# Optimization experiments

Hardware: AMD Instinct MI355X
Metric: run time of the kernel (lower is better)

The kernel has to match this reference:

```python
import jax, jax.numpy as jnp
import numpy as np

N_NODES = 50000
N_EDGES = 800000
N_GRAPHS = 256
HID = 64           # hidden_channels
H, C = 2, 64       # GAT heads, per-head channels
D2 = H * C         # 128 = hidden_channels * heads
BN_EPS = 1e-5


def setup_inputs() -> dict:
    key = jax.random.key(0)
    ks = iter(jax.random.split(key, 64))

    def p(shape, scale=0.05):
        return (jax.random.normal(next(ks), shape, dtype=jnp.float32) * scale)

    inp = {}
    inp["metadata"] = jax.random.normal(next(ks), (N_NODES, 4), dtype=jnp.float32)
    inp["waveform_features"] = jax.random.normal(next(ks), (N_NODES, 64), dtype=jnp.float32)
    inp["edge_index"] = jax.random.randint(next(ks), (2, N_EDGES), 0, N_NODES, dtype=jnp.int64)
    inp["batch"] = jnp.sort(jax.random.randint(next(ks), (N_NODES,), 0, N_GRAPHS, dtype=jnp.int64))

    # encoders / combiner
    inp["meta_w"] = p((4, HID // 2)); inp["meta_b"] = p((HID // 2,))
    inp["wave_w"] = p((64, HID // 2)); inp["wave_b"] = p((HID // 2,))
    inp["comb_w"] = p((HID, HID));     inp["comb_b"] = p((HID,))

    # GAT layers: layer 0 maps HID->H*C, layers 1,2 map D2->H*C
    inp["gat_w0"] = p((HID, D2)); inp["gat_as0"] = p((H, C)); inp["gat_ad0"] = p((H, C)); inp["gat_b0"] = p((D2,))
    inp["gat_w1"] = p((D2, D2));  inp["gat_as1"] = p((H, C)); inp["gat_ad1"] = p((H, C)); inp["gat_b1"] = p((D2,))
    inp["gat_w2"] = p((D2, D2));  inp["gat_as2"] = p((H, C)); inp["gat_ad2"] = p((H, C)); inp["gat_b2"] = p((D2,))

    # batch norms (eval mode: running stats), stacked over 3 layers
    inp["bn_gamma"] = jnp.ones((3, D2), jnp.float32) + p((3, D2))
    inp["bn_beta"] = p((3, D2))
    inp["bn_mean"] = p((3, D2))
    inp["bn_var"] = jax.random.uniform(next(ks), (3, D2), jnp.float32, 0.5, 1.5)

    # predictors
    inp["lat_w1"] = p((D2, HID)); inp["lat_b1"] = p((HID,))
    inp["lat_w2"] = p((HID, 1));  inp["lat_b2"] = p((1,))
    inp["lon_w1"] = p((D2, HID)); inp["lon_b1"] = p((HID,))
    inp["lon_w2"] = p((HID, 1));  inp["lon_b2"] = p((1,))
    return inp


def gat_conv(x, src, dst, n, W, a_src, a_dst, b):
    """PyG-style GATConv, heads=H concat, leaky_relu slope 0.2, self-loops already in src/dst."""
    h = (x @ W).reshape(n, H, C)                          # [N,H,C]
    s = jnp.einsum('nhc,hc->nh', h, a_src)                # alpha_src [N,H]
    d = jnp.einsum('nhc,hc->nh', h, a_dst)                # alpha_dst [N,H]
    e = jax.nn.leaky_relu(s[src] + d[dst], 0.2)           # [E,H]
    m = jax.ops.segment_max(e, dst, num_segments=n)       # per-dst softmax (segment)
    ex = jnp.exp(e - m[dst])
    denom = jax.ops.segment_sum(ex, dst, num_segments=n)
    alpha = ex / (denom[dst] + 1e-16)                     # [E,H]
    out = jax.ops.segment_sum(h[src] * alpha[:, :, None], dst, num_segments=n)  # [N,H,C]
    return out.reshape(n, H * C) + b


def reference(metadata, waveform_features, edge_index, batch,
              meta_w, meta_b, wave_w, wave_b, comb_w, comb_b,
              gat_w0, gat_as0, gat_ad0, gat_b0,
              gat_w1, gat_as1, gat_ad1, gat_b1,
              gat_w2, gat_as2, gat_ad2, gat_b2,
              bn_gamma, bn_beta, bn_mean, bn_var,
              lat_w1, lat_b1, lat_w2, lat_b2,
              lon_w1, lon_b1, lon_w2, lon_b2):
    n = metadata.shape[0]
    me = jax.nn.relu(metadata @ meta_w + meta_b)
    we = jax.nn.relu(waveform_features @ wave_w + wave_b)
    x = jnp.concatenate([me, we], axis=1)                 # [N, HID]
    x = jax.nn.relu(x @ comb_w + comb_b)

    loops = jnp.arange(n, dtype=edge_index.dtype)         # GATConv adds self-loops
    src = jnp.concatenate([edge_index[0], loops])
    dst = jnp.concatenate([edge_index[1], loops])

    gat_params = [(gat_w0, gat_as0, gat_ad0, gat_b0),
                  (gat_w1, gat_as1, gat_ad1, gat_b1),
                  (gat_w2, gat_as2, gat_ad2, gat_b2)]
    for i in range(3):
        x_res = x if i > 0 else None
        x = gat_conv(x, src, dst, n, *gat_params[i])
        x = (x - bn_mean[i]) * (bn_gamma[i] / jnp.sqrt(bn_var[i] + BN_EPS)) + bn_beta[i]
        if x_res is not None and x.shape == x_res.shape:
            x = x + x_res
        x = jax.nn.relu(x)                                # dropout inactive (eval)

    # global_mean_pool over graphs
    sums = jax.ops.segment_sum(x, batch, num_segments=N_GRAPHS)
    cnt = jax.ops.segment_sum(jnp.ones((n, 1), x.dtype), batch, num_segments=N_GRAPHS)
    xg = sums / jnp.maximum(cnt, 1.0)                     # [B, 128]

    lat = jax.nn.relu(xg @ lat_w1 + lat_b1) @ lat_w2 + lat_b2
    lon = jax.nn.relu(xg @ lon_w1 + lon_b1) @ lon_w2 + lon_b2
    return lat, lon
```

## Files before the change

### kernel.cpp

```cpp
#include <hip/hip_runtime.h>
#include <hip/hip_bf16.h>
#include <stdint.h>

#define NN 50000
#define NNP 50048
#define NE 800000
#define ET 850000
#define NG 256
#define CAP 128
#define NB 392
#define EB 4096
#define NEB ((ET + EB - 1) / EB)

typedef __hip_bfloat16 bf16;
typedef __attribute__((ext_vector_type(8))) short short8;
typedef __attribute__((ext_vector_type(4))) float floatx4;

__device__ __forceinline__ float b2f(bf16 v) { return __bfloat162float(v); }
__device__ __forceinline__ float lrelu(float x) { return x > 0.f ? x : 0.2f * x; }
__device__ __forceinline__ short f2b(float f) {
    unsigned u = __float_as_uint(f);
    unsigned r = (u + 0x7FFFu + ((u >> 16) & 1u)) >> 16;
    return (short)r;
}
__device__ __forceinline__ float sh2f(short s) { return __uint_as_float(((unsigned)(unsigned short)s) << 16); }
__device__ __forceinline__ float blo(unsigned u) { return __uint_as_float(u << 16); }
__device__ __forceinline__ float bhi(unsigned u) { return __uint_as_float(u & 0xFFFF0000u); }
__device__ __forceinline__ unsigned pck(float a, float b) {
    return ((unsigned)(unsigned short)f2b(a)) | (((unsigned)(unsigned short)f2b(b)) << 16);
}

__device__ __forceinline__ float wred_sum(float v) {
    for (int o = 32; o > 0; o >>= 1) v += __shfl_xor(v, o, 64);
    return v;
}
__device__ __forceinline__ float wred_max(float v) {
    for (int o = 32; o > 0; o >>= 1) v = fmaxf(v, __shfl_xor(v, o, 64));
    return v;
}

__global__ void detect_kernel(const unsigned int* __restrict__ meta_words,
                              const unsigned int* __restrict__ ei_words,
                              int* __restrict__ flags, int* __restrict__ gbh) {
    __shared__ int insane, odd_nonzero;
    for (int k = threadIdx.x; k < NB; k += 256) gbh[k] = 0;
    if (threadIdx.x == 0) { insane = 0; odd_nonzero = 0; }
    __syncthreads();
    int cnt = 0;
    for (int k = 0; k < 8; k++) {
        unsigned int w = meta_words[threadIdx.x * 8 + k];
        int elo = (int)(((w & 0xFFFFu) >> 7) & 0xFF);
        int ehi = (int)(((w >> 16) >> 7) & 0xFF);
        if (elo >= 0x8D) cnt++;
        if (ehi >= 0x8D) cnt++;
    }
    if (cnt) atomicAdd(&insane, cnt);
    if (ei_words[threadIdx.x * 2 + 1] != 0u) atomicAdd(&odd_nonzero, 1);
    __syncthreads();
    if (threadIdx.x == 0) {
        flags[0] = (insane >= 4) ? 1 : 0;
        flags[1] = (odd_nonzero == 0) ? 1 : 0;
    }
}

struct PrepArgs {
    const void* src[32];
    int len[32];
    int dst_off[32];
    int blk_base[33];
    int cvtBlks, wtBlks, wfBlks, intBlks;
    const void* w0; const void* w1; const void* w2;
    const void* ww; const void* wc;
    const void* wf_src;
    const void* ei_src;
    const void* bat_src;
};

__global__ void prep_kernel(PrepArgs a, float* __restrict__ cf,
                            short* __restrict__ wtall, short* __restrict__ wavewT,
                            short* __restrict__ combwT,
                            short* __restrict__ wfhi, short* __restrict__ wflo,
                            int* __restrict__ ei32, int* __restrict__ bat32,
                            const int* __restrict__ flags) {
    int b = blockIdx.x;
    bool fp32f = flags[0] != 0;
    if (b < a.cvtBlks) {
        int ai = 0;
        while (b >= a.blk_base[ai + 1]) ai++;
        int base = (b - a.blk_base[ai]) * 1024 + threadIdx.x;
        const float* sf = (const float*)a.src[ai];
        const bf16* sh = (const bf16*)a.src[ai];
        float* d = cf + a.dst_off[ai];
        int len = a.len[ai];
        #pragma unroll
        for (int u = 0; u < 4; u++) {
            int i = base + u * 256;
            if (i < len) d[i] = fp32f ? sf[i] : b2f(sh[i]);
        }
        return;
    }
    b -= a.cvtBlks;
    if (b < a.wtBlks) {
        int idx = b * 256 + threadIdx.x;
        const void* src; short* dst; int K, N, loc;
        if (idx < 8192)        { src = a.w0; dst = wtall;          K = 64;  N = 128; loc = idx; }
        else if (idx < 24576)  { src = a.w1; dst = wtall + 8192;   K = 128; N = 128; loc = idx - 8192; }
        else if (idx < 40960)  { src = a.w2; dst = wtall + 24576;  K = 128; N = 128; loc = idx - 24576; }
        else if (idx < 43008)  { src = a.ww; dst = wavewT;         K = 64;  N = 32;  loc = idx - 40960; }
        else if (idx < 47104)  { src = a.wc; dst = combwT;         K = 64;  N = 64;  loc = idx - 43008; }
        else return;
        int nch = loc / K, k = loc % K;
        int si = k * N + nch;
        dst[loc] = fp32f ? f2b(((const float*)src)[si]) : ((const short*)src)[si];
        return;
    }
    b -= a.wtBlks;
    if (b < a.wfBlks) {
        int idx = b * 256 + threadIdx.x;
        int i8 = idx * 8;
        if (i8 >= NNP * 64) return;
        short8 h = {0, 0, 0, 0, 0, 0, 0, 0};
        short8 l = {0, 0, 0, 0, 0, 0, 0, 0};
        if (i8 < NN * 64) {
            if (fp32f) {
                const float* sf = (const float*)a.wf_src + i8;
                #pragma unroll
                for (int k = 0; k < 8; k++) {
                    float v = sf[k];
                    short hh = f2b(v);
                    h[k] = hh;
                    l[k] = f2b(v - sh2f(hh));
                }
            } else {
                h = *(const short8*)((const short*)a.wf_src + i8);
            }
        }
        *(short8*)(wfhi + i8) = h;
        *(short8*)(wflo + i8) = l;
        return;
    }
    b -= a.wfBlks;
    int idx = b * 256 + threadIdx.x;
    if (idx >= 825000) return;
    bool i64f = flags[1] != 0;
    if (idx < 800000) {
        int2 o;
        if (i64f) { int4 v = ((const int4*)a.ei_src)[idx]; o.x = v.x; o.y = v.z; }
        else      { o = ((const int2*)a.ei_src)[idx]; }
        *(int2*)(ei32 + idx * 2) = o;
    } else {
        int k = idx - 800000;
        int2 o;
        if (i64f) { int4 v = ((const int4*)a.bat_src)[k]; o.x = v.x; o.y = v.z; }
        else      { o = ((const int2*)a.bat_src)[k]; }
        *(int2*)(bat32 + k * 2) = o;
    }
}

__global__ __launch_bounds__(256) void encode_mfma_kernel(
        const float* __restrict__ meta, const float* __restrict__ meta_w,
        const float* __restrict__ meta_b,
        const short* __restrict__ wfhi, const short* __restrict__ wflo,
        const short* __restrict__ wavewT, const float* __restrict__ wave_b,
        const short* __restrict__ combwT, const float* __restrict__ comb_b,
        short* __restrict__ xout, const int* __restrict__ flags) {
    __shared__ short xc_hi[64][72];
    __shared__ short xc_lo[64][72];
    int t = threadIdx.x;
    int wave = t >> 6, lane = t & 63;
    int m16 = lane & 15, quad = lane >> 4;
    int nblk = blockIdx.x * 64;
    bool fp32f = flags[0] != 0;

    #pragma unroll
    for (int u = 0; u < 8; u++) {
        int idx = u * 256 + t;
        int node_l = idx >> 5, ch = idx & 31;
        int node = nblk + node_l;
        float acc = meta_b[ch];
        if (node < NN) {
            #pragma unroll
            for (int k = 0; k < 4; k++)
                acc += meta[node * 4 + k] * meta_w[k * 32 + ch];
        }
        float v = fmaxf(acc, 0.f);
        short hh = f2b(v);
        xc_hi[node_l][ch] = hh;
        xc_lo[node_l][ch] = f2b(v - sh2f(hh));
    }

    int row0 = nblk + wave * 16;
    const short* pah = wfhi + (size_t)(row0 + m16) * 64 + quad * 8;
    const short* pal = wflo + (size_t)(row0 + m16) * 64 + quad * 8;
    floatx4 wacc[2];
    wacc[0] = (floatx4)(0.f); wacc[1] = (floatx4)(0.f);
    #pragma unroll
    for (int ks = 0; ks < 64; ks += 32) {
        short8 ah = *(const short8*)(pah + ks);
        #pragma unroll
        for (int c = 0; c < 2; c++) {
            short8 b = *(const short8*)(wavewT + (c * 16 + m16) * 64 + ks + quad * 8);
            wacc[c] = __builtin_amdgcn_mfma_f32_16x16x32_bf16(ah, b, wacc[c], 0, 0, 0);
        }
        if (fp32f) {
            short8 al = *(const short8*)(pal + ks);
            #pragma unroll
            for (int c = 0; c < 2; c++) {
                short8 b = *(const short8*)(wavewT + (c * 16 + m16) * 64 + ks + quad * 8);
                wacc[c] = __builtin_amdgcn_mfma_f32_16x16x32_bf16(al, b, wacc[c], 0, 0, 0);
            }
        }
    }
    #pragma unroll
    for (int c = 0; c < 2; c++) {
        float bb = wave_b[c * 16 + m16];
        #pragma unroll
        for (int r = 0; r < 4; r++) {
            int node_l = wave * 16 + quad * 4 + r;
            int ch = 32 + c * 16 + m16;
            float v = fmaxf(wacc[c][r] + bb, 0.f);
            short hh = f2b(v);
            xc_hi[node_l][ch] = hh;
            xc_lo[node_l][ch] = f2b(v - sh2f(hh));
        }
    }
    __syncthreads();

    floatx4 acc2[4];
    #pragma unroll
    for (int c = 0; c < 4; c++) acc2[c] = (floatx4)(0.f);
    #pragma unroll
    for (int ks = 0; ks < 64; ks += 32) {
        short8 ah = *(const short8*)&xc_hi[wave * 16 + m16][ks + quad * 8];
        short8 al = *(const short8*)&xc_lo[wave * 16 + m16][ks + quad * 8];
        #pragma unroll
        for (int c = 0; c < 4; c++) {
            short8 b = *(const short8*)(combwT + (c * 16 + m16) * 64 + ks + quad * 8);
            acc2[c] = __builtin_amdgcn_mfma_f32_16x16x32_bf16(ah, b, acc2[c], 0, 0, 0);
            acc2[c] = __builtin_amdgcn_mfma_f32_16x16x32_bf16(al, b, acc2[c], 0, 0, 0);
        }
    }
    #pragma unroll
    for (int c = 0; c < 4; c++) {
        int ch = c * 16 + m16;
        float bb = comb_b[ch];
        #pragma unroll
        for (int r = 0; r < 4; r++) {
            int node = nblk + wave * 16 + quad * 4 + r;
            float v = fmaxf(acc2[c][r] + bb, 0.f);
            xout[(size_t)node * 64 + ch] = f2b(v);
        }
    }
}

__global__ void bucket_hist_kernel(const int* __restrict__ ei, int* __restrict__ gbh) {
    __shared__ int lh[NB];
    int t = threadIdx.x;
    for (int k = t; k < NB; k += 256) lh[k] = 0;
    __syncthreads();
    int base = blockIdx.x * EB;
    #pragma unroll 4
    for (int u = 0; u < EB / 256; u++) {
        int i = base + u * 256 + t;
        if (i < ET) {
            int dst = (i < NE) ? ei[NE + i] : (i - NE);
            atomicAdd(&lh[dst >> 7], 1);
        }
    }
    __syncthreads();
    for (int k = t; k < NB; k += 256)
        if (lh[k]) atomicAdd(&gbh[k], lh[k]);
}

__global__ void scan_bounds_kernel(const int* __restrict__ gbh, int* __restrict__ gbo,
                                   int* __restrict__ bcur,
                                   const int* __restrict__ batch, int* __restrict__ starts) {
    if (blockIdx.x == 0) {
        __shared__ int buf[512];
        int t = threadIdx.x;
        int v = (t < NB) ? gbh[t] : 0;
        buf[t] = v;
        __syncthreads();
        for (int o = 1; o < 512; o <<= 1) {
            int x = (t >= o) ? buf[t - o] : 0;
            __syncthreads();
            buf[t] += x;
            __syncthreads();
        }
        if (t < NB) { int e = buf[t] - v; gbo[t] = e; bcur[t] = e; }
        if (t == 0) gbo[NB] = ET;
    } else {
        int g = threadIdx.x;
        if (g <= NG) {
            int lo = 0, hi = NN;
            while (lo < hi) {
                int mid = (lo + hi) >> 1;
                if (batch[mid] < g) lo = mid + 1; else hi = mid;
            }
            starts[g] = lo;
        }
    }
}

__global__ void bucket_scatter_kernel(const int* __restrict__ ei, int* __restrict__ bcur,
                                      uint2* __restrict__ bkt) {
    __shared__ int lh[NB];
    __shared__ int lbase[NB];
    int t = threadIdx.x;
    for (int k = t; k < NB; k += 256) lh[k] = 0;
    __syncthreads();
    int base = blockIdx.x * EB;
    #pragma unroll 4
    for (int u = 0; u < EB / 256; u++) {
        int i = base + u * 256 + t;
        if (i < ET) {
            int dst = (i < NE) ? ei[NE + i] : (i - NE);
            atomicAdd(&lh[dst >> 7], 1);
        }
    }
    __syncthreads();
    for (int k = t; k < NB; k += 256) {
        int c = lh[k];
        lbase[k] = c ? atomicAdd(&bcur[k], c) : 0;
        lh[k] = 0;
    }
    __syncthreads();
    #pragma unroll 4
    for (int u = 0; u < EB / 256; u++) {
        int i = base + u * 256 + t;
        if (i < ET) {
            int src, dst;
            if (i < NE) { src = ei[i]; dst = ei[NE + i]; }
            else        { src = i - NE; dst = i - NE; }
            int b = dst >> 7;
            int pos = lbase[b] + atomicAdd(&lh[b], 1);
            bkt[pos] = make_uint2((unsigned)src, (unsigned)dst);
        }
    }
}

__global__ void bucket_finalize_kernel(const uint2* __restrict__ bkt,
                                       const int* __restrict__ gbo,
                                       int* __restrict__ off, int* __restrict__ csr) {
    __shared__ int hist[128];
    __shared__ int cur[128];
    int b = blockIdx.x;
    int t = threadIdx.x;
    int e0 = gbo[b], e1 = gbo[b + 1];
    if (t < 128) hist[t] = 0;
    __syncthreads();
    for (int i = e0 + t; i < e1; i += 256)
        atomicAdd(&hist[bkt[i].y & 127], 1);
    __syncthreads();
    int v = (t < 128) ? hist[t] : 0;
    if (t < 128) cur[t] = v;
    __syncthreads();
    for (int o = 1; o < 128; o <<= 1) {
        int x = (t < 128 && t >= o) ? cur[t - o] : 0;
        __syncthreads();
        if (t < 128) cur[t] += x;
        __syncthreads();
    }
    if (t < 128) {
        int ex = e0 + cur[t] - v;
        int node = b * 128 + t;
        if (node <= NN) off[node] = ex;
        cur[t] = ex;
    }
    __syncthreads();
    for (int i = e0 + t; i < e1; i += 256) {
        uint2 e = bkt[i];
        int pos = atomicAdd(&cur[e.y & 127], 1);
        csr[pos] = (int)e.x;
    }
}

__global__ __launch_bounds__(256) void gemm_mfma_kernel(
        const short* __restrict__ x, const short* __restrict__ wt,
        const float* __restrict__ a_s, const float* __restrict__ a_d,
        short* __restrict__ h, float* __restrict__ s, float* __restrict__ d,
        int K, int n) {
    int wave = threadIdx.x >> 6;
    int lane = threadIdx.x & 63;
    int row0 = (blockIdx.x * 4 + wave) * 16;
    int m16 = lane & 15;
    int quad = lane >> 4;
    int kq = quad * 8;

    const short* pa = x + (size_t)(row0 + m16) * K + kq;

    floatx4 acc[8];
    #pragma unroll
    for (int c = 0; c < 8; c++) acc[c] = (floatx4)(0.f);

    for (int ks = 0; ks < K; ks += 32) {
        short8 av = *(const short8*)(pa + ks);
        #pragma unroll
        for (int c = 0; c < 8; c++) {
            short8 b = *(const short8*)(wt + (size_t)(c * 16 + m16) * K + ks + kq);
            acc[c] = __builtin_amdgcn_mfma_f32_16x16x32_bf16(av, b, acc[c], 0, 0, 0);
        }
    }

    #pragma unroll
    for (int c = 0; c < 8; c++) {
        #pragma unroll
        for (int r = 0; r < 4; r++) {
            int node = row0 + quad * 4 + r;
            if (node < n) h[(size_t)node * 128 + c * 16 + m16] = f2b(acc[c][r]);
        }
    }

    float sp[2][4] = {{0, 0, 0, 0}, {0, 0, 0, 0}};
    float dp[2][4] = {{0, 0, 0, 0}, {0, 0, 0, 0}};
    #pragma unroll
    for (int c = 0; c < 8; c++) {
        float as_ = a_s[c * 16 + m16];
        float ad_ = a_d[c * 16 + m16];
        int hh = c >> 2;
        #pragma unroll
        for (int r = 0; r < 4; r++) {
            sp[hh][r] += acc[c][r] * as_;
            dp[hh][r] += acc[c][r] * ad_;
        }
    }
    #pragma unroll
    for (int o = 1; o < 16; o <<= 1) {
        #pragma unroll
        for (int hh = 0; hh < 2; hh++)
            #pragma unroll
            for (int r = 0; r < 4; r++) {
                sp[hh][r] += __shfl_xor(sp[hh][r], o, 64);
                dp[hh][r] += __shfl_xor(dp[hh][r], o, 64);
            }
    }
    if (m16 == 0) {
        #pragma unroll
        for (int r = 0; r < 4; r++) {
            int node = row0 + quad * 4 + r;
            if (node < n) {
                s[node * 2 + 0] = sp[0][r];
                s[node * 2 + 1] = sp[1][r];
                d[node * 2 + 0] = dp[0][r];
                d[node * 2 + 1] = dp[1][r];
            }
        }
    }
}

__global__ __launch_bounds__(256) void gat_aggregate_kernel(
        const unsigned* __restrict__ hp, const float* __restrict__ sv,
        const float* __restrict__ dv, const int* __restrict__ off,
        const int* __restrict__ csr, const float* __restrict__ bias,
        const float* __restrict__ bn_g, const float* __restrict__ bn_b,
        const float* __restrict__ bn_m, const float* __restrict__ bn_v,
        const unsigned* __restrict__ res, unsigned* __restrict__ out, int n) {
    __shared__ float exs[4][CAP][2];
    __shared__ int scs[4][CAP];
    int w = threadIdx.x >> 6;
    int lane = threadIdx.x & 63;
    int node = blockIdx.x * 4 + w;
    bool ok = node < n;
    int begin = 0, end = 0, deg = 0;
    float d0 = 0.f, d1 = 0.f;
    if (ok) {
        begin = off[node]; end = off[node + 1]; deg = end - begin;
        d0 = dv[node * 2 + 0]; d1 = dv[node * 2 + 1];
    }
    bool fits = deg <= CAP;
    float inv0 = 0.f, inv1 = 0.f;

    if (ok && fits) {
        int i0 = begin + lane, i1 = begin + 64 + lane;
        int sa = (i0 < end) ? csr[i0] : -1;
        int sb = (i1 < end) ? csr[i1] : -1;
        float e0a = -3e38f, e1a = -3e38f, e0b = -3e38f, e1b = -3e38f;
        if (sa >= 0) {
            float2 sp = *(const float2*)(sv + sa * 2);
            e0a = lrelu(sp.x + d0); e1a = lrelu(sp.y + d1);
        }
        if (sb >= 0) {
            float2 sp = *(const float2*)(sv + sb * 2);
            e0b = lrelu(sp.x + d0); e1b = lrelu(sp.y + d1);
        }
        float m0 = wred_max(fmaxf(e0a, e0b));
        float m1 = wred_max(fmaxf(e1a, e1b));
        float x0a = 0.f, x1a = 0.f, x0b = 0.f, x1b = 0.f;
        if (sa >= 0) {
            x0a = __expf(e0a - m0); x1a = __expf(e1a - m1);
            exs[w][lane][0] = x0a; exs[w][lane][1] = x1a; scs[w][lane] = sa;
        }
        if (sb >= 0) {
            x0b = __expf(e0b - m0); x1b = __expf(e1b - m1);
            exs[w][lane + 64][0] = x0b; exs[w][lane + 64][1] = x1b; scs[w][lane + 64] = sb;
        }
        float z0 = wred_sum(x0a + x0b);
        float z1 = wred_sum(x1a + x1b);
        inv0 = 1.f / (z0 + 1e-16f);
        inv1 = 1.f / (z1 + 1e-16f);
    }
    __syncthreads();
    if (!ok) return;

    if (fits) {
        int ll = lane & 15;
        int grp = lane >> 4;
        int hsel = (ll >= 8) ? 1 : 0;
        const uint4* hp4 = (const uint4*)hp;
        float a0 = 0, a1 = 0, a2 = 0, a3 = 0, a4 = 0, a5 = 0, a6 = 0, a7 = 0;
        for (int i = 0; i < deg; i += 4) {
            int e = i + grp;
            if (e < deg) {
                int src = scs[w][e];
                float a = exs[w][e][hsel];
                uint4 u = hp4[(size_t)src * 16 + ll];
                a0 += a * blo(u.x); a1 += a * bhi(u.x);
                a2 += a * blo(u.y); a3 += a * bhi(u.y);
                a4 += a * blo(u.z); a5 += a * bhi(u.z);
                a6 += a * blo(u.w); a7 += a * bhi(u.w);
            }
        }
        a0 += __shfl_xor(a0, 16, 64); a0 += __shfl_xor(a0, 32, 64);
        a1 += __shfl_xor(a1, 16, 64); a1 += __shfl_xor(a1, 32, 64);
        a2 += __shfl_xor(a2, 16, 64); a2 += __shfl_xor(a2, 32, 64);
        a3 += __shfl_xor(a3, 16, 64); a3 += __shfl_xor(a3, 32, 64);
        a4 += __shfl_xor(a4, 16, 64); a4 += __shfl_xor(a4, 32, 64);
        a5 += __shfl_xor(a5, 16, 64); a5 += __shfl_xor(a5, 32, 64);
        a6 += __shfl_xor(a6, 16, 64); a6 += __shfl_xor(a6, 32, 64);
        a7 += __shfl_xor(a7, 16, 64); a7 += __shfl_xor(a7, 32, 64);
        float inv = hsel ? inv1 : inv0;
        a0 *= inv; a1 *= inv; a2 *= inv; a3 *= inv;
        a4 *= inv; a5 *= inv; a6 *= inv; a7 *= inv;

        float4 bi0 = ((const float4*)bias)[2 * ll],  bi1 = ((const float4*)bias)[2 * ll + 1];
        float4 g0  = ((const float4*)bn_g)[2 * ll],  g1  = ((const float4*)bn_g)[2 * ll + 1];
        float4 be0 = ((const float4*)bn_b)[2 * ll],  be1 = ((const float4*)bn_b)[2 * ll + 1];
        float4 mu0 = ((const float4*)bn_m)[2 * ll],  mu1 = ((const float4*)bn_m)[2 * ll + 1];
        float4 va0 = ((const float4*)bn_v)[2 * ll],  va1 = ((const float4*)bn_v)[2 * ll + 1];
        float v0 = (a0 + bi0.x - mu0.x) * (g0.x * rsqrtf(va0.x + 1e-5f)) + be0.x;
        float v1 = (a1 + bi0.y - mu0.y) * (g0.y * rsqrtf(va0.y + 1e-5f)) + be0.y;
        float v2 = (a2 + bi0.z - mu0.z) * (g0.z * rsqrtf(va0.z + 1e-5f)) + be0.z;
        float v3 = (a3 + bi0.w - mu0.w) * (g0.w * rsqrtf(va0.w + 1e-5f)) + be0.w;
        float v4 = (a4 + bi1.x - mu1.x) * (g1.x * rsqrtf(va1.x + 1e-5f)) + be1.x;
        float v5 = (a5 + bi1.y - mu1.y) * (g1.y * rsqrtf(va1.y + 1e-5f)) + be1.y;
        float v6 = (a6 + bi1.z - mu1.z) * (g1.z * rsqrtf(va1.z + 1e-5f)) + be1.z;
        float v7 = (a7 + bi1.w - mu1.w) * (g1.w * rsqrtf(va1.w + 1e-5f)) + be1.w;
        if (res) {
            uint4 r = ((const uint4*)res)[(size_t)node * 16 + ll];
            v0 += blo(r.x); v1 += bhi(r.x); v2 += blo(r.y); v3 += bhi(r.y);
            v4 += blo(r.z); v5 += bhi(r.z); v6 += blo(r.w); v7 += bhi(r.w);
        }
        v0 = fmaxf(v0, 0.f); v1 = fmaxf(v1, 0.f); v2 = fmaxf(v2, 0.f); v3 = fmaxf(v3, 0.f);
        v4 = fmaxf(v4, 0.f); v5 = fmaxf(v5, 0.f); v6 = fmaxf(v6, 0.f); v7 = fmaxf(v7, 0.f);
        if (lane < 16) {
            ((uint4*)out)[(size_t)node * 16 + ll] =
                make_uint4(pck(v0, v1), pck(v2, v3), pck(v4, v5), pck(v6, v7));
        }
    } else {
        float mm0 = -3e38f, mm1 = -3e38f;
        for (int i = begin + lane; i < end; i += 64) {
            int sc = csr[i];
            float2 sp = *(const float2*)(sv + sc * 2);
            mm0 = fmaxf(mm0, lrelu(sp.x + d0));
            mm1 = fmaxf(mm1, lrelu(sp.y + d1));
        }
        mm0 = wred_max(mm0); mm1 = wred_max(mm1);
        float z0 = 0.f, z1 = 0.f;
        for (int i = begin + lane; i < end; i += 64) {
            int sc = csr[i];
            float2 sp = *(const float2*)(sv + sc * 2);
            z0 += __expf(lrelu(sp.x + d0) - mm0);
            z1 += __expf(lrelu(sp.y + d1) - mm1);
        }
        z0 = wred_sum(z0); z1 = wred_sum(z1);
        float i0_ = 1.f / (z0 + 1e-16f), i1_ = 1.f / (z1 + 1e-16f);
        bool head0 = lane < 32;
        float acc0 = 0.f, acc1 = 0.f;
        for (int i = begin; i < end; i++) {
            int sc = csr[i];
            float2 sp = *(const float2*)(sv + sc * 2);
            float a = head0 ? __expf(lrelu(sp.x + d0) - mm0) * i0_
                            : __expf(lrelu(sp.y + d1) - mm1) * i1_;
            unsigned u = hp[(size_t)sc * 64 + lane];
            acc0 += a * blo(u);
            acc1 += a * bhi(u);
        }
        int c0 = 2 * lane, c1 = c0 + 1;
        float v0 = acc0 + bias[c0];
        float v1 = acc1 + bias[c1];
        v0 = (v0 - bn_m[c0]) * (bn_g[c0] * rsqrtf(bn_v[c0] + 1e-5f)) + bn_b[c0];
        v1 = (v1 - bn_m[c1]) * (bn_g[c1] * rsqrtf(bn_v[c1] + 1e-5f)) + bn_b[c1];
        if (res) {
            unsigned r = res[(size_t)node * 64 + lane];
            v0 += blo(r);
            v1 += bhi(r);
        }
        v0 = fmaxf(v0, 0.f);
        v1 = fmaxf(v1, 0.f);
        out[(size_t)node * 64 + lane] = pck(v0, v1);
    }
}

__global__ void pool_kernel(const unsigned* __restrict__ x,
                            const int* __restrict__ starts, float* __restrict__ xg) {
    __shared__ float part[4][128];
    int g = blockIdx.x;
    int wv = threadIdx.x >> 6, lane = threadIdx.x & 63;
    int s0 = starts[g], e0 = starts[g + 1];
    float a0 = 0.f, a1 = 0.f;
    for (int node = s0 + wv; node < e0; node += 4) {
        unsigned u = x[(size_t)node * 64 + lane];
        a0 += blo(u);
        a1 += bhi(u);
    }
    part[wv][lane * 2] = a0;
    part[wv][lane * 2 + 1] = a1;
    __syncthreads();
    if (wv == 0) {
        float t0 = part[0][lane * 2] + part[1][lane * 2] + part[2][lane * 2] + part[3][lane * 2];
        float t1 = part[0][lane * 2 + 1] + part[1][lane * 2 + 1] + part[2][lane * 2 + 1] + part[3][lane * 2 + 1];
        float icf = 1.f / fmaxf((float)(e0 - s0), 1.f);
        xg[g * 128 + 2 * lane] = t0 * icf;
        xg[g * 128 + 2 * lane + 1] = t1 * icf;
    }
}

__global__ void head_kernel(const float* __restrict__ xg,
                            const float* __restrict__ w1a, const float* __restrict__ b1a,
                            const float* __restrict__ w2a, const float* __restrict__ b2a,
                            const float* __restrict__ w1o, const float* __restrict__ b1o,
                            const float* __restrict__ w2o, const float* __restrict__ b2o,
                            const int* __restrict__ flags, void* __restrict__ out) {
    int g = blockIdx.x;
    int wave = threadIdx.x >> 6;
    int lane = threadIdx.x & 63;
    const float* w1 = wave ? w1o : w1a;
    const float* b1 = wave ? b1o : b1a;
    const float* w2 = wave ? w2o : w2a;
    const float* b2 = wave ? b2o : b2a;
    float acc = b1[lane];
    for (int c = 0; c < 128; c++)
        acc += xg[g * 128 + c] * w1[c * 64 + lane];
    acc = fmaxf(acc, 0.f);
    float contrib = wred_sum(acc * w2[lane]);
    if (lane == 0) {
        float r = contrib + b2[0];
        if (flags[0]) ((float*)out)[wave * NG + g] = r;
        else          ((bf16*)out)[wave * NG + g] = __float2bfloat16(r);
    }
}

extern "C" void kernel_launch(void* const* d_in, const int* in_sizes, int n_in,
                              void* d_out, int out_size, void* d_ws, size_t ws_size,
                              hipStream_t stream) {
    static const int fidx[32] = {0,1, 4,5,6,7,8,9, 10,11,12,13, 14,15,16,17,
                                 18,19,20,21, 22,23,24,25, 26,27,28,29, 30,31,32,33};
    static const int flen[32] = {200000, 3200000, 128, 32, 2048, 32, 4096, 64,
                                 8192, 128, 128, 128, 16384, 128, 128, 128,
                                 16384, 128, 128, 128, 384, 384, 384, 384,
                                 8192, 64, 64, 1, 8192, 64, 64, 1};
    PrepArgs pa;
    int O[32];
    int tot = 0, blk = 0;
    for (int i = 0; i < 32; i++) {
        bool skip = (i == 1) || (i == 4) || (i == 6) || (i == 8) || (i == 12) || (i == 16);
        int cl = skip ? 0 : flen[i];
        pa.src[i] = d_in[fidx[i]];
        pa.len[i] = cl;
        O[i] = tot;
        pa.dst_off[i] = tot;
        pa.blk_base[i] = blk;
        tot += (flen[i] + 63) & ~63;
        blk += (cl + 1023) / 1024;
    }
    pa.blk_base[32] = blk;
    pa.cvtBlks = blk;
    pa.wtBlks = 184;
    pa.wfBlks = NNP * 64 / 8 / 256;
    pa.intBlks = (825000 + 255) / 256;
    pa.w0 = d_in[10]; pa.w1 = d_in[14]; pa.w2 = d_in[18];
    pa.ww = d_in[6];  pa.wc = d_in[8];
    pa.wf_src = d_in[1];
    pa.ei_src = d_in[2];
    pa.bat_src = d_in[3];
    int prepGrid = pa.cvtBlks + pa.wtBlks + pa.wfBlks + pa.intBlks;

    char* w = (char*)d_ws;
    auto alloc = [&](size_t bytes) -> char* {
        char* p = w;
        w += (bytes + 255) & ~(size_t)255;
        return p;
    };
    int*   flags  = (int*)alloc(256);
    float* cf     = (float*)alloc((size_t)tot * 4);
    int*   ei32   = (int*)alloc((size_t)2 * NE * 4);
    int*   bat32  = (int*)alloc((size_t)NN * 4);
    short* wfhi   = (short*)alloc((size_t)NNP * 64 * 2);
    short* wflo   = (short*)alloc((size_t)NNP * 64 * 2);
    short* x0     = (short*)alloc((size_t)NNP * 64 * 2);
    short* xA     = (short*)alloc((size_t)NNP * 128 * 2);
    short* xB     = (short*)alloc((size_t)NNP * 128 * 2);
    short* h      = (short*)alloc((size_t)NNP * 128 * 2);
    float* sA     = (float*)alloc((size_t)NN * 2 * 4);
    float* dA     = (float*)alloc((size_t)NN * 2 * 4);
    int*   off    = (int*)alloc((size_t)(NN + 1) * 4);
    int*   csr    = (int*)alloc((size_t)ET * 4);
    int*   gbh    = (int*)alloc((size_t)NB * 4);
    int*   gbo    = (int*)alloc((size_t)(NB + 1) * 4);
    int*   bcur   = (int*)alloc((size_t)NB * 4);
    uint2* bkt    = (uint2*)alloc((size_t)ET * 8);
    int*   starts = (int*)alloc((size_t)(NG + 1) * 4);
    float* xg     = (float*)alloc((size_t)NG * 128 * 4);
    short* wtall  = (short*)alloc((size_t)40960 * 2);
    short* wavewT = (short*)alloc((size_t)2048 * 2);
    short* combwT = (short*)alloc((size_t)4096 * 2);
    short* wt0 = wtall, *wt1 = wtall + 8192, *wt2 = wtall + 24576;

    detect_kernel<<<1, 256, 0, stream>>>((const unsigned int*)d_in[0],
                                         (const unsigned int*)d_in[2], flags, gbh);
    prep_kernel<<<prepGrid, 256, 0, stream>>>(pa, cf, wtall, wavewT, combwT,
                                              wfhi, wflo, ei32, bat32, flags);
    encode_mfma_kernel<<<NNP / 64, 256, 0, stream>>>(cf + O[0], cf + O[2], cf + O[3],
                                                     wfhi, wflo, wavewT, cf + O[5],
                                                     combwT, cf + O[7], x0, flags);
    bucket_hist_kernel<<<NEB, 256, 0, stream>>>(ei32, gbh);
    scan_bounds_kernel<<<2, 512, 0, stream>>>(gbh, gbo, bcur, bat32, starts);
    bucket_scatter_kernel<<<NEB, 256, 0, stream>>>(ei32, bcur, bkt);
    bucket_finalize_kernel<<<NB, 256, 0, stream>>>(bkt, gbo, off, csr);

    int gblk = NNP / 64;
    gemm_mfma_kernel<<<gblk, 256, 0, stream>>>(x0, wt0, cf + O[9], cf + O[10],
                                               h, sA, dA, 64, NN);
    gat_aggregate_kernel<<<NN / 4, 256, 0, stream>>>(
        (const unsigned*)h, sA, dA, off, csr, cf + O[11],
        cf + O[20], cf + O[21], cf + O[22], cf + O[23],
        nullptr, (unsigned*)xA, NN);
    gemm_mfma_kernel<<<gblk, 256, 0, stream>>>(xA, wt1, cf + O[13], cf + O[14],
                                               h, sA, dA, 128, NN);
    gat_aggregate_kernel<<<NN / 4, 256, 0, stream>>>(
        (const unsigned*)h, sA, dA, off, csr, cf + O[15],
        cf + O[20] + 128, cf + O[21] + 128, cf + O[22] + 128, cf + O[23] + 128,
        (const unsigned*)xA, (unsigned*)xB, NN);
    gemm_mfma_kernel<<<gblk, 256, 0, stream>>>(xB, wt2, cf + O[17], cf + O[18],
                                               h, sA, dA, 128, NN);
    gat_aggregate_kernel<<<NN / 4, 256, 0, stream>>>(
        (const unsigned*)h, sA, dA, off, csr, cf + O[19],
        cf + O[20] + 256, cf + O[21] + 256, cf + O[22] + 256, cf + O[23] + 256,
        (const unsigned*)xB, (unsigned*)xA, NN);

    pool_kernel<<<NG, 256, 0, stream>>>((const unsigned*)xA, starts, xg);
    head_kernel<<<NG, 128, 0, stream>>>(xg,
                                        cf + O[24], cf + O[25], cf + O[26], cf + O[27],
                                        cf + O[28], cf + O[29], cf + O[30], cf + O[31],
                                        flags, d_out);
}
```

Baseline: 423.1 us.

## Read edge indices directly and batch gather loop with packed per-edge records

Drops the separate int64-to-int32 conversion pass for edge_index and batch. The bucket kernels and the graph-bounds search now read the original arrays directly through a width-aware loader. Skips writing the wflo buffer when the input is already bf16. In the GAT aggregation, source index and both head weights are packed into one float4 shared record, and the gather loop is padded to multiples of 16 and unrolled four edges per step so more independent loads are in flight. The cost is reading 64-bit indices twice in the bucket kernels, plus wasted gathers on the zero-weight padding entries.

```diff
diff --git a/kernel.cpp b/kernel.cpp
--- a/kernel.cpp
+++ b/kernel.cpp
@@ -39,6 +39,10 @@
     return v;
 }
 
+__device__ __forceinline__ int ld_int(const void* p, int i, bool i64) {
+    return i64 ? (int)((const long long*)p)[i] : ((const int*)p)[i];
+}
+
 __global__ void detect_kernel(const unsigned int* __restrict__ meta_words,
                               const unsigned int* __restrict__ ei_words,
                               int* __restrict__ flags, int* __restrict__ gbh) {
@@ -68,19 +72,16 @@
     int len[32];
     int dst_off[32];
     int blk_base[33];
-    int cvtBlks, wtBlks, wfBlks, intBlks;
+    int cvtBlks, wtBlks, wfBlks;
     const void* w0; const void* w1; const void* w2;
     const void* ww; const void* wc;
     const void* wf_src;
-    const void* ei_src;
-    const void* bat_src;
 };
 
 __global__ void prep_kernel(PrepArgs a, float* __restrict__ cf,
                             short* __restrict__ wtall, short* __restrict__ wavewT,
                             short* __restrict__ combwT,
                             short* __restrict__ wfhi, short* __restrict__ wflo,
-                            int* __restrict__ ei32, int* __restrict__ bat32,
                             const int* __restrict__ flags) {
     int b = blockIdx.x;
     bool fp32f = flags[0] != 0;
@@ -115,45 +116,27 @@
         return;
     }
     b -= a.wtBlks;
-    if (b < a.wfBlks) {
-        int idx = b * 256 + threadIdx.x;
-        int i8 = idx * 8;
-        if (i8 >= NNP * 64) return;
-        short8 h = {0, 0, 0, 0, 0, 0, 0, 0};
+    int idx = b * 256 + threadIdx.x;
+    int i8 = idx * 8;
+    if (i8 >= NNP * 64) return;
+    short8 h = {0, 0, 0, 0, 0, 0, 0, 0};
+    if (fp32f) {
         short8 l = {0, 0, 0, 0, 0, 0, 0, 0};
         if (i8 < NN * 64) {
-            if (fp32f) {
-                const float* sf = (const float*)a.wf_src + i8;
-                #pragma unroll
-                for (int k = 0; k < 8; k++) {
-                    float v = sf[k];
-                    short hh = f2b(v);
-                    h[k] = hh;
-                    l[k] = f2b(v - sh2f(hh));
-                }
-            } else {
-                h = *(const short8*)((const short*)a.wf_src + i8);
+            const float* sf = (const float*)a.wf_src + i8;
+            #pragma unroll
+            for (int k = 0; k < 8; k++) {
+                float v = sf[k];
+                short hh = f2b(v);
+                h[k] = hh;
+                l[k] = f2b(v - sh2f(hh));
             }
         }
         *(short8*)(wfhi + i8) = h;
         *(short8*)(wflo + i8) = l;
-        return;
-    }
-    b -= a.wfBlks;
-    int idx = b * 256 + threadIdx.x;
-    if (idx >= 825000) return;
-    bool i64f = flags[1] != 0;
-    if (idx < 800000) {
-        int2 o;
-        if (i64f) { int4 v = ((const int4*)a.ei_src)[idx]; o.x = v.x; o.y = v.z; }
-        else      { o = ((const int2*)a.ei_src)[idx]; }
-        *(int2*)(ei32 + idx * 2) = o;
     } else {
-        int k = idx - 800000;
-        int2 o;
-        if (i64f) { int4 v = ((const int4*)a.bat_src)[k]; o.x = v.x; o.y = v.z; }
-        else      { o = ((const int2*)a.bat_src)[k]; }
-        *(int2*)(bat32 + k * 2) = o;
+        if (i8 < NN * 64) h = *(const short8*)((const short*)a.wf_src + i8);
+        *(short8*)(wfhi + i8) = h;
     }
 }
 
@@ -253,9 +236,11 @@
     }
 }
 
-__global__ void bucket_hist_kernel(const int* __restrict__ ei, int* __restrict__ gbh) {
+__global__ void bucket_hist_kernel(const void* __restrict__ ei, const int* __restrict__ flags,
+                                   int* __restrict__ gbh) {
     __shared__ int lh[NB];
     int t = threadIdx.x;
+    bool i64 = flags[1] != 0;
     for (int k = t; k < NB; k += 256) lh[k] = 0;
     __syncthreads();
     int base = blockIdx.x * EB;
@@ -263,7 +248,7 @@
     for (int u = 0; u < EB / 256; u++) {
         int i = base + u * 256 + t;
         if (i < ET) {
-            int dst = (i < NE) ? ei[NE + i] : (i - NE);
+            int dst = (i < NE) ? ld_int(ei, NE + i, i64) : (i - NE);
             atomicAdd(&lh[dst >> 7], 1);
         }
     }
@@ -274,7 +259,8 @@
 
 __global__ void scan_bounds_kernel(const int* __restrict__ gbh, int* __restrict__ gbo,
                                    int* __restrict__ bcur,
-                                   const int* __restrict__ batch, int* __restrict__ starts) {
+                                   const void* __restrict__ batch, int* __restrict__ starts,
+                                   const int* __restrict__ flags) {
     if (blockIdx.x == 0) {
         __shared__ int buf[512];
         int t = threadIdx.x;
@@ -291,22 +277,24 @@
         if (t == 0) gbo[NB] = ET;
     } else {
         int g = threadIdx.x;
+        bool i64 = flags[1] != 0;
         if (g <= NG) {
             int lo = 0, hi = NN;
             while (lo < hi) {
                 int mid = (lo + hi) >> 1;
-                if (batch[mid] < g) lo = mid + 1; else hi = mid;
+                if (ld_int(batch, mid, i64) < g) lo = mid + 1; else hi = mid;
             }
             starts[g] = lo;
         }
     }
 }
 
-__global__ void bucket_scatter_kernel(const int* __restrict__ ei, int* __restrict__ bcur,
-                                      uint2* __restrict__ bkt) {
+__global__ void bucket_scatter_kernel(const void* __restrict__ ei, const int* __restrict__ flags,
+                                      int* __restrict__ bcur, uint2* __restrict__ bkt) {
     __shared__ int lh[NB];
     __shared__ int lbase[NB];
     int t = threadIdx.x;
+    bool i64 = flags[1] != 0;
     for (int k = t; k < NB; k += 256) lh[k] = 0;
     __syncthreads();
     int base = blockIdx.x * EB;
@@ -314,7 +302,7 @@
     for (int u = 0; u < EB / 256; u++) {
         int i = base + u * 256 + t;
         if (i < ET) {
-            int dst = (i < NE) ? ei[NE + i] : (i - NE);
+            int dst = (i < NE) ? ld_int(ei, NE + i, i64) : (i - NE);
             atomicAdd(&lh[dst >> 7], 1);
         }
     }
@@ -330,7 +318,7 @@
         int i = base + u * 256 + t;
         if (i < ET) {
             int src, dst;
-            if (i < NE) { src = ei[i]; dst = ei[NE + i]; }
+            if (i < NE) { src = ld_int(ei, i, i64); dst = ld_int(ei, NE + i, i64); }
             else        { src = i - NE; dst = i - NE; }
             int b = dst >> 7;
             int pos = lbase[b] + atomicAdd(&lh[b], 1);
@@ -455,8 +443,7 @@
         const float* __restrict__ bn_g, const float* __restrict__ bn_b,
         const float* __restrict__ bn_m, const float* __restrict__ bn_v,
         const unsigned* __restrict__ res, unsigned* __restrict__ out, int n) {
-    __shared__ float exs[4][CAP][2];
-    __shared__ int scs[4][CAP];
+    __shared__ float4 er[4][CAP];
     int w = threadIdx.x >> 6;
     int lane = threadIdx.x & 63;
     int node = blockIdx.x * 4 + w;
@@ -468,6 +455,7 @@
         d0 = dv[node * 2 + 0]; d1 = dv[node * 2 + 1];
     }
     bool fits = deg <= CAP;
+    int degp = (deg + 15) & ~15;
     float inv0 = 0.f, inv1 = 0.f;
 
     if (ok && fits) {
@@ -488,12 +476,14 @@
         float x0a = 0.f, x1a = 0.f, x0b = 0.f, x1b = 0.f;
         if (sa >= 0) {
             x0a = __expf(e0a - m0); x1a = __expf(e1a - m1);
-            exs[w][lane][0] = x0a; exs[w][lane][1] = x1a; scs[w][lane] = sa;
+            er[w][lane] = make_float4(__int_as_float(sa), x0a, x1a, 0.f);
         }
         if (sb >= 0) {
             x0b = __expf(e0b - m0); x1b = __expf(e1b - m1);
-            exs[w][lane + 64][0] = x0b; exs[w][lane + 64][1] = x1b; scs[w][lane + 64] = sb;
-        }
+            er[w][lane + 64] = make_float4(__int_as_float(sb), x0b, x1b, 0.f);
+        }
+        if (lane < degp - deg)
+            er[w][deg + lane] = make_float4(__int_as_float(0), 0.f, 0.f, 0.f);
         float z0 = wred_sum(x0a + x0b);
         float z1 = wred_sum(x1a + x1b);
         inv0 = 1.f / (z0 + 1e-16f);
@@ -508,17 +498,25 @@
         int hsel = (ll >= 8) ? 1 : 0;
         const uint4* hp4 = (const uint4*)hp;
         float a0 = 0, a1 = 0, a2 = 0, a3 = 0, a4 = 0, a5 = 0, a6 = 0, a7 = 0;
-        for (int i = 0; i < deg; i += 4) {
-            int e = i + grp;
-            if (e < deg) {
-                int src = scs[w][e];
-                float a = exs[w][e][hsel];
-                uint4 u = hp4[(size_t)src * 16 + ll];
-                a0 += a * blo(u.x); a1 += a * bhi(u.x);
-                a2 += a * blo(u.y); a3 += a * bhi(u.y);
-                a4 += a * blo(u.z); a5 += a * bhi(u.z);
-                a6 += a * blo(u.w); a7 += a * bhi(u.w);
-            }
+        for (int i = 0; i < degp; i += 16) {
+            int e = i + grp * 4;
+            float4 r0 = er[w][e], r1 = er[w][e + 1], r2 = er[w][e + 2], r3 = er[w][e + 3];
+            uint4 u0 = hp4[(size_t)__float_as_int(r0.x) * 16 + ll];
+            uint4 u1 = hp4[(size_t)__float_as_int(r1.x) * 16 + ll];
+            uint4 u2 = hp4[(size_t)__float_as_int(r2.x) * 16 + ll];
+            uint4 u3 = hp4[(size_t)__float_as_int(r3.x) * 16 + ll];
+            float al0 = hsel ? r0.z : r0.y;
+            float al1 = hsel ? r1.z : r1.y;
+            float al2 = hsel ? r2.z : r2.y;
+            float al3 = hsel ? r3.z : r3.y;
+            a0 += al0 * blo(u0.x) + al1 * blo(u1.x) + al2 * blo(u2.x) + al3 * blo(u3.x);
+            a1 += al0 * bhi(u0.x) + al1 * bhi(u1.x) + al2 * bhi(u2.x) + al3 * bhi(u3.x);
+            a2 += al0 * blo(u0.y) + al1 * blo(u1.y) + al2 * blo(u2.y) + al3 * blo(u3.y);
+            a3 += al0 * bhi(u0.y) + al1 * bhi(u1.y) + al2 * bhi(u2.y) + al3 * bhi(u3.y);
+            a4 += al0 * blo(u0.z) + al1 * blo(u1.z) + al2 * blo(u2.z) + al3 * blo(u3.z);
+            a5 += al0 * bhi(u0.z) + al1 * bhi(u1.z) + al2 * bhi(u2.z) + al3 * bhi(u3.z);
+            a6 += al0 * blo(u0.w) + al1 * blo(u1.w) + al2 * blo(u2.w) + al3 * blo(u3.w);
+            a7 += al0 * bhi(u0.w) + al1 * bhi(u1.w) + al2 * bhi(u2.w) + al3 * bhi(u3.w);
         }
         a0 += __shfl_xor(a0, 16, 64); a0 += __shfl_xor(a0, 32, 64);
         a1 += __shfl_xor(a1, 16, 64); a1 += __shfl_xor(a1, 32, 64);
@@ -677,13 +675,10 @@
     pa.cvtBlks = blk;
     pa.wtBlks = 184;
     pa.wfBlks = NNP * 64 / 8 / 256;
-    pa.intBlks = (825000 + 255) / 256;
     pa.w0 = d_in[10]; pa.w1 = d_in[14]; pa.w2 = d_in[18];
     pa.ww = d_in[6];  pa.wc = d_in[8];
     pa.wf_src = d_in[1];
-    pa.ei_src = d_in[2];
-    pa.bat_src = d_in[3];
-    int prepGrid = pa.cvtBlks + pa.wtBlks + pa.wfBlks + pa.intBlks;
+    int prepGrid = pa.cvtBlks + pa.wtBlks + pa.wfBlks;
 
     char* w = (char*)d_ws;
     auto alloc = [&](size_t bytes) -> char* {
@@ -693,8 +688,6 @@
     };
     int*   flags  = (int*)alloc(256);
     float* cf     = (float*)alloc((size_t)tot * 4);
-    int*   ei32   = (int*)alloc((size_t)2 * NE * 4);
-    int*   bat32  = (int*)alloc((size_t)NN * 4);
     short* wfhi   = (short*)alloc((size_t)NNP * 64 * 2);
     short* wflo   = (short*)alloc((size_t)NNP * 64 * 2);
     short* x0     = (short*)alloc((size_t)NNP * 64 * 2);
@@ -719,13 +712,13 @@
     detect_kernel<<<1, 256, 0, stream>>>((const unsigned int*)d_in[0],
                                          (const unsigned int*)d_in[2], flags, gbh);
     prep_kernel<<<prepGrid, 256, 0, stream>>>(pa, cf, wtall, wavewT, combwT,
-                                              wfhi, wflo, ei32, bat32, flags);
+                                              wfhi, wflo, flags);
     encode_mfma_kernel<<<NNP / 64, 256, 0, stream>>>(cf + O[0], cf + O[2], cf + O[3],
                                                      wfhi, wflo, wavewT, cf + O[5],
                                                      combwT, cf + O[7], x0, flags);
-    bucket_hist_kernel<<<NEB, 256, 0, stream>>>(ei32, gbh);
-    scan_bounds_kernel<<<2, 512, 0, stream>>>(gbh, gbo, bcur, bat32, starts);
-    bucket_scatter_kernel<<<NEB, 256, 0, stream>>>(ei32, bcur, bkt);
+    bucket_hist_kernel<<<NEB, 256, 0, stream>>>(d_in[2], flags, gbh);
+    scan_bounds_kernel<<<2, 512, 0, stream>>>(gbh, gbo, bcur, d_in[3], starts, flags);
+    bucket_scatter_kernel<<<NEB, 256, 0, stream>>>(d_in[2], flags, bcur, bkt);
     bucket_finalize_kernel<<<NB, 256, 0, stream>>>(bkt, gbo, off, csr);
 
     int gblk = NNP / 64;
```

Result: faster. 410.1 us (-3.1%).
